# Optimization experiments

Hardware: AMD Instinct MI355X
Metric: run time of the kernel (lower is better)

The kernel has to match this reference:

```python
import jax, jax.numpy as jnp
import numpy as np

MARGIN = 1.0

def _pairwise_sqdist(z):
    # ||zi - zj||^2 = ||zi||^2 + ||zj||^2 - 2 zi.zj
    sq = jnp.sum(z * z, axis=-1)  # [N]
    d2 = sq[:, None] + sq[None, :] - 2.0 * (z @ z.T)
    return jnp.maximum(d2, 0.0)

def _safe_sqrt(d2):
    # sqrt with well-defined gradient at 0 (matches cdist values; diag = 0)
    pos = d2 > 0.0
    return jnp.where(pos, jnp.sqrt(jnp.where(pos, d2, 1.0)), 0.0)

def setup_inputs() -> dict:
    key = jax.random.key(0)
    k1, k2 = jax.random.split(key)
    z = jax.random.normal(k1, (8192, 128), dtype=jnp.float32)
    labels = jax.random.randint(k2, (8192,), 0, 100, dtype=jnp.int64)
    return {"z": z, "labels": labels}

def reference(z, labels):
    d2 = _pairwise_sqdist(z)              # [N, N] squared distances
    dist = _safe_sqrt(d2)                 # [N, N] distances
    label_eq = labels[:, None] == labels[None, :]
    pos = jnp.where(label_eq, d2, 0.0)
    neg = jnp.where(label_eq, 0.0, jnp.square(jax.nn.relu(MARGIN - dist)))
    return jnp.mean(pos + neg)
```

## Files before the change

### kernel.cpp

```cpp
#include <hip/hip_runtime.h>
#include <stdint.h>


#define NROWS 8192
#define DIMK  128
#define NB    64
#define NBLK  (NB * (NB + 1) / 2)

typedef __attribute__((ext_vector_type(4))) float f32x4;
typedef __attribute__((ext_vector_type(2))) long long2v;

#define AS_GLOBAL __attribute__((address_space(1)))
#define AS_LDS    __attribute__((address_space(3)))

__global__ __launch_bounds__(256) void prep_kernel(
    const float* __restrict__ z, unsigned char* __restrict__ zb,
    float* __restrict__ sq) {
  int lane = threadIdx.x & 63, wave = threadIdx.x >> 6;
  int row = (blockIdx.x << 2) + wave;
  float2 x = ((const float2*)(z + (size_t)row * DIMK))[lane];
  int pk = __builtin_amdgcn_cvt_pk_fp8_f32(x.x, x.y, 0, false);
  float r0 = __builtin_amdgcn_cvt_f32_fp8(pk, 0);
  float r1 = __builtin_amdgcn_cvt_f32_fp8(pk, 1);
  float s = r0 * r0 + r1 * r1;
  int k = lane << 1;
  int p = (((k >> 3) & 3) << 5) + ((k >> 5) << 3) + (k & 7);
  *(unsigned short*)(zb + (size_t)row * DIMK + p) = (unsigned short)(pk & 0xFFFF);
  #pragma unroll
  for (int off = 32; off; off >>= 1) s += __shfl_down(s, off);
  if (lane == 0) sq[row] = s;
}

__global__ __launch_bounds__(512, 4) void loss_kernel(
    const unsigned char* __restrict__ zb, const float* __restrict__ sq,
    const int* __restrict__ labels, float* __restrict__ partials) {
  __shared__ __align__(16) unsigned char ldsA[16384];
  __shared__ __align__(16) unsigned char ldsB[16384];
  __shared__ __align__(16) float sqAl[128];
  __shared__ __align__(16) float sqBl[128];
  __shared__ __align__(16) int   laAl[128];
  __shared__ __align__(16) int   laBl[128];
  __shared__ float red[8];

  int tid = threadIdx.x, lane = tid & 63, wave = tid >> 6;

  int bid = blockIdx.x;
  #define TRI(rr) ((rr) * NB - ((rr) * ((rr) - 1)) / 2)
  int r = (int)(((float)(2 * NB + 1) -
                 sqrtf((float)((2 * NB + 1) * (2 * NB + 1) - 8 * bid))) * 0.5f);
  if (r < 0) r = 0; if (r > NB - 1) r = NB - 1;
  while (TRI(r + 1) <= bid) ++r;
  while (TRI(r) > bid) --r;
  int bi = r, bj = bid - TRI(r) + r;

  const unsigned char* Ab = zb + (((size_t)bi << 7) * DIMK);
  const unsigned char* Bb = zb + (((size_t)bj << 7) * DIMK);
  #pragma unroll
  for (int t = 0; t < 2; ++t) {
    int L0 = (t << 9) + (wave << 6);
    int L  = L0 + lane;
    int rw = L >> 3;
    int c  = (L & 7) ^ (rw & 7);
    __builtin_amdgcn_global_load_lds(
        (const AS_GLOBAL void*)(uintptr_t)(Ab + rw * DIMK + (c << 4)),
        (AS_LDS void*)(uintptr_t)(ldsA + (size_t)L0 * 16), 16, 0, 0);
    __builtin_amdgcn_global_load_lds(
        (const AS_GLOBAL void*)(uintptr_t)(Bb + rw * DIMK + (c << 4)),
        (AS_LDS void*)(uintptr_t)(ldsB + (size_t)L0 * 16), 16, 0, 0);
  }
  if (tid < 128) {
    sqAl[tid] = sq[(bi << 7) + tid];
    laAl[tid] = labels[(bi << 7) + tid];
  } else if (tid < 256) {
    int t2 = tid & 127;
    sqBl[t2] = sq[(bj << 7) + t2];
    laBl[t2] = labels[(bj << 7) + t2];
  }
  asm volatile("s_waitcnt vmcnt(0)" ::: "memory");
  __syncthreads();

  int wm = wave >> 1, wn = wave & 1;
  int lc = lane & 15;
  int q  = lane >> 4;
  int x7 = lc & 7;
  long a[2][4], b[4][4];
  #pragma unroll
  for (int i = 0; i < 2; ++i) {
    const unsigned char* base = ldsA + ((wm << 5) + (i << 4) + lc) * 128;
    long2v lo = *(const long2v*)(base + ((((q << 1)    ) ^ x7) << 4));
    long2v hi = *(const long2v*)(base + ((((q << 1) + 1) ^ x7) << 4));
    a[i][0] = lo.x; a[i][1] = lo.y; a[i][2] = hi.x; a[i][3] = hi.y;
  }
  #pragma unroll
  for (int j = 0; j < 4; ++j) {
    const unsigned char* base = ldsB + ((wn << 6) + (j << 4) + lc) * 128;
    long2v lo = *(const long2v*)(base + ((((q << 1)    ) ^ x7) << 4));
    long2v hi = *(const long2v*)(base + ((((q << 1) + 1) ^ x7) << 4));
    b[j][0] = lo.x; b[j][1] = lo.y; b[j][2] = hi.x; b[j][3] = hi.y;
  }
  f32x4 acc[2][4] = {};
  #pragma unroll
  for (int ks = 0; ks < 4; ++ks)
    #pragma unroll
    for (int i = 0; i < 2; ++i)
      #pragma unroll
      for (int j = 0; j < 4; ++j)
        acc[i][j] = __builtin_amdgcn_mfma_f32_16x16x32_fp8_fp8(
            a[i][ks], b[j][ks], acc[i][j], 0, 0, 0);

  int r0 = q << 2;
  float sn_[4]; int ln_[4];
  #pragma unroll
  for (int j = 0; j < 4; ++j) {
    int n = (wn << 6) + (j << 4) + lc;
    sn_[j] = sqBl[n]; ln_[j] = laBl[n];
  }
  float ps0 = 0.f, ps1 = 0.f, ps2 = 0.f, ps3 = 0.f;
  #pragma unroll
  for (int i = 0; i < 2; ++i) {
    int mb = (wm << 5) + (i << 4) + r0;
    f32x4 sm4 = *(const f32x4*)&sqAl[mb];
    int4  lm4 = *(const int4*)&laAl[mb];
    #pragma unroll
    for (int j = 0; j < 4; ++j) {
      float d0  = fmaf(-2.f, acc[i][j][0], sm4[0] + sn_[j]);
      float d1  = fmaf(-2.f, acc[i][j][1], sm4[1] + sn_[j]);
      float d2_ = fmaf(-2.f, acc[i][j][2], sm4[2] + sn_[j]);
      float d3  = fmaf(-2.f, acc[i][j][3], sm4[3] + sn_[j]);
      float mn = fminf(fminf(d0, d1), fminf(d2_, d3));
      if (__builtin_expect(__any(mn < 1.f), 0)) {
        float dc, t;
        dc = fmaxf(d0, 0.f);  t = fmaxf(1.f - sqrtf(dc), 0.f);
        ps0 += (lm4.x == ln_[j]) ? dc : t * t;
        dc = fmaxf(d1, 0.f);  t = fmaxf(1.f - sqrtf(dc), 0.f);
        ps1 += (lm4.y == ln_[j]) ? dc : t * t;
        dc = fmaxf(d2_, 0.f); t = fmaxf(1.f - sqrtf(dc), 0.f);
        ps2 += (lm4.z == ln_[j]) ? dc : t * t;
        dc = fmaxf(d3, 0.f);  t = fmaxf(1.f - sqrtf(dc), 0.f);
        ps3 += (lm4.w == ln_[j]) ? dc : t * t;
      } else {
        ps0 += (lm4.x == ln_[j]) ? d0  : 0.f;
        ps1 += (lm4.y == ln_[j]) ? d1  : 0.f;
        ps2 += (lm4.z == ln_[j]) ? d2_ : 0.f;
        ps3 += (lm4.w == ln_[j]) ? d3  : 0.f;
      }
    }
  }
  float psum = (ps0 + ps1) + (ps2 + ps3);
  float w = (bi == bj) ? 1.f : 2.f;
  psum *= w * (1.f / (8192.f * 8192.f));

  #pragma unroll
  for (int off = 32; off; off >>= 1) psum += __shfl_down(psum, off);
  if (lane == 0) red[wave] = psum;
  __syncthreads();
  if (tid == 0) {
    float s = 0.f;
    #pragma unroll
    for (int k = 0; k < 8; ++k) s += red[k];
    partials[bid] = s;
  }
}

__global__ __launch_bounds__(256) void reduce_kernel(
    const float* __restrict__ partials, float* __restrict__ out) {
  int tid = threadIdx.x, lane = tid & 63, wave = tid >> 6;
  float s = 0.f;
  for (int k = tid; k < NBLK; k += 256) s += partials[k];
  #pragma unroll
  for (int off = 32; off; off >>= 1) s += __shfl_down(s, off);
  __shared__ float red[4];
  if (lane == 0) red[wave] = s;
  __syncthreads();
  if (tid == 0) out[0] = red[0] + red[1] + red[2] + red[3];
}

extern "C" void kernel_launch(void* const* d_in, const int* in_sizes, int n_in,
                              void* d_out, int out_size, void* d_ws, size_t ws_size,
                              hipStream_t stream) {
  const float* z      = (const float*)d_in[0];
  const int*   labels = (const int*)d_in[1];
  float*       out    = (float*)d_out;
  unsigned char* zb   = (unsigned char*)d_ws;
  char* p = (char*)d_ws + (size_t)NROWS * DIMK;
  float* sq       = (float*)p;
  float* partials = (float*)(p + NROWS * 4);

  prep_kernel<<<NROWS / 4, 256, 0, stream>>>(z, zb, sq);
  loss_kernel<<<NBLK, 512, 0, stream>>>(zb, sq, labels, partials);
  reduce_kernel<<<1, 256, 0, stream>>>(partials, out);
}
```

Baseline: 76.27 us.

## Fuse final reduction via last-block atomic, enlarge per-wave tiles, widen prep

Prep now converts four floats per thread, packing them into fp8 with a 32-bit store, and also resets a completion counter. The loss kernel drops to 256 threads per block, so each wave computes a 64x64 tile with K split into two passes to keep register use in check. The near-margin sqrt path is now decided once per wave rather than per 16x16 subtile. The separate reduce kernel is gone: the last block to finish, detected with an atomic counter, sums the partials, saving a launch at the cost of a fence plus atomic in every block.

```diff
diff --git a/kernel.cpp b/kernel.cpp
--- a/kernel.cpp
+++ b/kernel.cpp
@@ -15,32 +15,39 @@
 
 __global__ __launch_bounds__(256) void prep_kernel(
     const float* __restrict__ z, unsigned char* __restrict__ zb,
-    float* __restrict__ sq) {
-  int lane = threadIdx.x & 63, wave = threadIdx.x >> 6;
-  int row = (blockIdx.x << 2) + wave;
-  float2 x = ((const float2*)(z + (size_t)row * DIMK))[lane];
-  int pk = __builtin_amdgcn_cvt_pk_fp8_f32(x.x, x.y, 0, false);
-  float r0 = __builtin_amdgcn_cvt_f32_fp8(pk, 0);
-  float r1 = __builtin_amdgcn_cvt_f32_fp8(pk, 1);
-  float s = r0 * r0 + r1 * r1;
-  int k = lane << 1;
-  int p = (((k >> 3) & 3) << 5) + ((k >> 5) << 3) + (k & 7);
-  *(unsigned short*)(zb + (size_t)row * DIMK + p) = (unsigned short)(pk & 0xFFFF);
-  #pragma unroll
-  for (int off = 32; off; off >>= 1) s += __shfl_down(s, off);
-  if (lane == 0) sq[row] = s;
+    float* __restrict__ sq, unsigned int* __restrict__ counter) {
+  if (blockIdx.x == 0 && threadIdx.x == 0) *counter = 0;
+  int tid = threadIdx.x;
+  int row = (blockIdx.x << 3) + (tid >> 5);
+  int c32 = tid & 31;
+  float4 x = ((const float4*)(z + (size_t)row * DIMK))[c32];
+  int u = __builtin_amdgcn_cvt_pk_fp8_f32(x.x, x.y, 0, false);
+  u     = __builtin_amdgcn_cvt_pk_fp8_f32(x.z, x.w, u, true);
+  float r0 = __builtin_amdgcn_cvt_f32_fp8(u, 0);
+  float r1 = __builtin_amdgcn_cvt_f32_fp8(u, 1);
+  float r2 = __builtin_amdgcn_cvt_f32_fp8(u, 2);
+  float r3 = __builtin_amdgcn_cvt_f32_fp8(u, 3);
+  float s = (r0 * r0 + r1 * r1) + (r2 * r2 + r3 * r3);
+  int k0 = c32 << 2;
+  int p = (((k0 >> 3) & 3) << 5) + ((k0 >> 5) << 3) + (k0 & 7);
+  *(uint32_t*)(zb + (size_t)row * DIMK + p) = (uint32_t)u;
+  #pragma unroll
+  for (int off = 16; off; off >>= 1) s += __shfl_down(s, off, 32);
+  if (c32 == 0) sq[row] = s;
 }
 
-__global__ __launch_bounds__(512, 4) void loss_kernel(
+__global__ __launch_bounds__(256, 4) void loss_kernel(
     const unsigned char* __restrict__ zb, const float* __restrict__ sq,
-    const int* __restrict__ labels, float* __restrict__ partials) {
+    const int* __restrict__ labels, float* __restrict__ partials,
+    unsigned int* __restrict__ counter, float* __restrict__ out) {
   __shared__ __align__(16) unsigned char ldsA[16384];
   __shared__ __align__(16) unsigned char ldsB[16384];
   __shared__ __align__(16) float sqAl[128];
   __shared__ __align__(16) float sqBl[128];
   __shared__ __align__(16) int   laAl[128];
   __shared__ __align__(16) int   laBl[128];
-  __shared__ float red[8];
+  __shared__ float red[4];
+  __shared__ int lastFlag;
 
   int tid = threadIdx.x, lane = tid & 63, wave = tid >> 6;
 
@@ -56,8 +63,8 @@
   const unsigned char* Ab = zb + (((size_t)bi << 7) * DIMK);
   const unsigned char* Bb = zb + (((size_t)bj << 7) * DIMK);
   #pragma unroll
-  for (int t = 0; t < 2; ++t) {
-    int L0 = (t << 9) + (wave << 6);
+  for (int t = 0; t < 4; ++t) {
+    int L0 = (t << 8) + (wave << 6);
     int L  = L0 + lane;
     int rw = L >> 3;
     int c  = (L & 7) ^ (rw & 7);
@@ -71,7 +78,7 @@
   if (tid < 128) {
     sqAl[tid] = sq[(bi << 7) + tid];
     laAl[tid] = labels[(bi << 7) + tid];
-  } else if (tid < 256) {
+  } else {
     int t2 = tid & 127;
     sqBl[t2] = sq[(bj << 7) + t2];
     laBl[t2] = labels[(bj << 7) + t2];
@@ -83,30 +90,31 @@
   int lc = lane & 15;
   int q  = lane >> 4;
   int x7 = lc & 7;
-  long a[2][4], b[4][4];
-  #pragma unroll
-  for (int i = 0; i < 2; ++i) {
-    const unsigned char* base = ldsA + ((wm << 5) + (i << 4) + lc) * 128;
-    long2v lo = *(const long2v*)(base + ((((q << 1)    ) ^ x7) << 4));
-    long2v hi = *(const long2v*)(base + ((((q << 1) + 1) ^ x7) << 4));
-    a[i][0] = lo.x; a[i][1] = lo.y; a[i][2] = hi.x; a[i][3] = hi.y;
-  }
-  #pragma unroll
-  for (int j = 0; j < 4; ++j) {
-    const unsigned char* base = ldsB + ((wn << 6) + (j << 4) + lc) * 128;
-    long2v lo = *(const long2v*)(base + ((((q << 1)    ) ^ x7) << 4));
-    long2v hi = *(const long2v*)(base + ((((q << 1) + 1) ^ x7) << 4));
-    b[j][0] = lo.x; b[j][1] = lo.y; b[j][2] = hi.x; b[j][3] = hi.y;
-  }
-  f32x4 acc[2][4] = {};
-  #pragma unroll
-  for (int ks = 0; ks < 4; ++ks)
-    #pragma unroll
-    for (int i = 0; i < 2; ++i)
+  f32x4 acc[4][4] = {};
+  #pragma unroll
+  for (int kp = 0; kp < 2; ++kp) {
+    long2v a[4], b[4];
+    #pragma unroll
+    for (int i = 0; i < 4; ++i)
+      a[i] = *(const long2v*)(ldsA + ((wm << 6) + (i << 4) + lc) * 128 +
+                              ((((q << 1) + kp) ^ x7) << 4));
+    #pragma unroll
+    for (int j = 0; j < 4; ++j)
+      b[j] = *(const long2v*)(ldsB + ((wn << 6) + (j << 4) + lc) * 128 +
+                              ((((q << 1) + kp) ^ x7) << 4));
+    #pragma unroll
+    for (int i = 0; i < 4; ++i)
       #pragma unroll
       for (int j = 0; j < 4; ++j)
         acc[i][j] = __builtin_amdgcn_mfma_f32_16x16x32_fp8_fp8(
-            a[i][ks], b[j][ks], acc[i][j], 0, 0, 0);
+            a[i].x, b[j].x, acc[i][j], 0, 0, 0);
+    #pragma unroll
+    for (int i = 0; i < 4; ++i)
+      #pragma unroll
+      for (int j = 0; j < 4; ++j)
+        acc[i][j] = __builtin_amdgcn_mfma_f32_16x16x32_fp8_fp8(
+            a[i].y, b[j].y, acc[i][j], 0, 0, 0);
+  }
 
   int r0 = q << 2;
   float sn_[4]; int ln_[4];
@@ -116,9 +124,10 @@
     sn_[j] = sqBl[n]; ln_[j] = laBl[n];
   }
   float ps0 = 0.f, ps1 = 0.f, ps2 = 0.f, ps3 = 0.f;
-  #pragma unroll
-  for (int i = 0; i < 2; ++i) {
-    int mb = (wm << 5) + (i << 4) + r0;
+  float mnall = 1e30f;
+  #pragma unroll
+  for (int i = 0; i < 4; ++i) {
+    int mb = (wm << 6) + (i << 4) + r0;
     f32x4 sm4 = *(const f32x4*)&sqAl[mb];
     int4  lm4 = *(const int4*)&laAl[mb];
     #pragma unroll
@@ -127,22 +136,35 @@
       float d1  = fmaf(-2.f, acc[i][j][1], sm4[1] + sn_[j]);
       float d2_ = fmaf(-2.f, acc[i][j][2], sm4[2] + sn_[j]);
       float d3  = fmaf(-2.f, acc[i][j][3], sm4[3] + sn_[j]);
-      float mn = fminf(fminf(d0, d1), fminf(d2_, d3));
-      if (__builtin_expect(__any(mn < 1.f), 0)) {
+      mnall = fminf(mnall, fminf(fminf(d0, d1), fminf(d2_, d3)));
+      ps0 += (lm4.x == ln_[j]) ? d0  : 0.f;
+      ps1 += (lm4.y == ln_[j]) ? d1  : 0.f;
+      ps2 += (lm4.z == ln_[j]) ? d2_ : 0.f;
+      ps3 += (lm4.w == ln_[j]) ? d3  : 0.f;
+    }
+  }
+  if (__builtin_expect(__any(mnall < 1.f), 0)) {
+    ps0 = ps1 = ps2 = ps3 = 0.f;
+    #pragma unroll
+    for (int i = 0; i < 4; ++i) {
+      int mb = (wm << 6) + (i << 4) + r0;
+      f32x4 sm4 = *(const f32x4*)&sqAl[mb];
+      int4  lm4 = *(const int4*)&laAl[mb];
+      #pragma unroll
+      for (int j = 0; j < 4; ++j) {
         float dc, t;
-        dc = fmaxf(d0, 0.f);  t = fmaxf(1.f - sqrtf(dc), 0.f);
+        dc = fmaxf(fmaf(-2.f, acc[i][j][0], sm4[0] + sn_[j]), 0.f);
+        t = fmaxf(1.f - sqrtf(dc), 0.f);
         ps0 += (lm4.x == ln_[j]) ? dc : t * t;
-        dc = fmaxf(d1, 0.f);  t = fmaxf(1.f - sqrtf(dc), 0.f);
+        dc = fmaxf(fmaf(-2.f, acc[i][j][1], sm4[1] + sn_[j]), 0.f);
+        t = fmaxf(1.f - sqrtf(dc), 0.f);
         ps1 += (lm4.y == ln_[j]) ? dc : t * t;
-        dc = fmaxf(d2_, 0.f); t = fmaxf(1.f - sqrtf(dc), 0.f);
+        dc = fmaxf(fmaf(-2.f, acc[i][j][2], sm4[2] + sn_[j]), 0.f);
+        t = fmaxf(1.f - sqrtf(dc), 0.f);
         ps2 += (lm4.z == ln_[j]) ? dc : t * t;
-        dc = fmaxf(d3, 0.f);  t = fmaxf(1.f - sqrtf(dc), 0.f);
+        dc = fmaxf(fmaf(-2.f, acc[i][j][3], sm4[3] + sn_[j]), 0.f);
+        t = fmaxf(1.f - sqrtf(dc), 0.f);
         ps3 += (lm4.w == ln_[j]) ? dc : t * t;
-      } else {
-        ps0 += (lm4.x == ln_[j]) ? d0  : 0.f;
-        ps1 += (lm4.y == ln_[j]) ? d1  : 0.f;
-        ps2 += (lm4.z == ln_[j]) ? d2_ : 0.f;
-        ps3 += (lm4.w == ln_[j]) ? d3  : 0.f;
       }
     }
   }
@@ -155,24 +177,22 @@
   if (lane == 0) red[wave] = psum;
   __syncthreads();
   if (tid == 0) {
+    partials[bid] = (red[0] + red[1]) + (red[2] + red[3]);
+    __threadfence();
+    unsigned int tk = atomicAdd(counter, 1u);
+    lastFlag = (tk == NBLK - 1);
+  }
+  __syncthreads();
+  if (lastFlag) {
+    __threadfence();
     float s = 0.f;
-    #pragma unroll
-    for (int k = 0; k < 8; ++k) s += red[k];
-    partials[bid] = s;
-  }
-}
-
-__global__ __launch_bounds__(256) void reduce_kernel(
-    const float* __restrict__ partials, float* __restrict__ out) {
-  int tid = threadIdx.x, lane = tid & 63, wave = tid >> 6;
-  float s = 0.f;
-  for (int k = tid; k < NBLK; k += 256) s += partials[k];
-  #pragma unroll
-  for (int off = 32; off; off >>= 1) s += __shfl_down(s, off);
-  __shared__ float red[4];
-  if (lane == 0) red[wave] = s;
-  __syncthreads();
-  if (tid == 0) out[0] = red[0] + red[1] + red[2] + red[3];
+    for (int k = tid; k < NBLK; k += 256) s += partials[k];
+    #pragma unroll
+    for (int off = 32; off; off >>= 1) s += __shfl_down(s, off);
+    if (lane == 0) red[wave] = s;
+    __syncthreads();
+    if (tid == 0) out[0] = (red[0] + red[1]) + (red[2] + red[3]);
+  }
 }
 
 extern "C" void kernel_launch(void* const* d_in, const int* in_sizes, int n_in,
@@ -183,10 +203,10 @@
   float*       out    = (float*)d_out;
   unsigned char* zb   = (unsigned char*)d_ws;
   char* p = (char*)d_ws + (size_t)NROWS * DIMK;
-  float* sq       = (float*)p;
-  float* partials = (float*)(p + NROWS * 4);
-
-  prep_kernel<<<NROWS / 4, 256, 0, stream>>>(z, zb, sq);
-  loss_kernel<<<NBLK, 512, 0, stream>>>(zb, sq, labels, partials);
-  reduce_kernel<<<1, 256, 0, stream>>>(partials, out);
+  float* sq             = (float*)p;
+  float* partials       = (float*)(p + NROWS * 4);
+  unsigned int* counter = (unsigned int*)(p + NROWS * 4 + NBLK * 4);
+
+  prep_kernel<<<NROWS / 8, 256, 0, stream>>>(z, zb, sq, counter);
+  loss_kernel<<<NBLK, 256, 0, stream>>>(zb, sq, labels, partials, counter, out);
 }
```

Result: slower. 175.6 us (+130.3%).
